# Kernel optimization log

Measured on AMD Instinct MI355X. Metric: run time of the kernel, lower is better.

Reference implementation:

```python
import jax, jax.numpy as jnp
import numpy as np

B = 128      # trees per batch
D = 10       # tree depth (perfect binary tree)
L = 2 ** D   # leaves per tree
V = 50000    # vocab
E = 300      # embed size
C = 5        # num classes


def setup_inputs() -> dict:
    key = jax.random.key(0)
    k0, k1, k2, k3 = jax.random.split(key, 4)
    return {
        "word_ids": jax.random.randint(k0, (B, L), 0, V),
        "embedding": jax.random.normal(k1, (V, E), jnp.float32) * 0.02,
        "W_w": jax.random.normal(k2, (E, 2 * E), jnp.float32) * (1.0 / np.sqrt(2 * E)),
        "W_b": jnp.zeros((E,), jnp.float32),
        "P_w": jax.random.normal(k3, (C, E), jnp.float32) * (1.0 / np.sqrt(E)),
        "P_b": jnp.zeros((C,), jnp.float32),
    }


def reference(word_ids, embedding, W_w, W_b, P_w, P_b):
    # Leaf nodes: relu(Embedding(word))  -> [B, L, E]
    h = jax.nn.relu(embedding[word_ids])
    # projection of every node (torch Linear: x @ W.T + b)
    logits = [jnp.einsum("bne,ce->bnc", h, P_w) + P_b]
    # Combine same-depth sibling pairs level by level (D fixed levels).
    for _ in range(D):
        pair = jnp.concatenate([h[:, 0::2], h[:, 1::2]], axis=-1)  # [B, n/2, 2E]
        h = jax.nn.relu(jnp.einsum("bnf,ef->bne", pair, W_w) + W_b)  # [B, n/2, E]
        logits.append(jnp.einsum("bne,ce->bnc", h, P_w) + P_b)
    # All node logits, leaves first then each internal level up to the root.
    return jnp.concatenate(logits, axis=1)  # [B, 2L-1, C]
```

## Files before the change

### kernel.cpp

```cpp
#include <hip/hip_runtime.h>
#include <hip/hip_bf16.h>

#define B_ 128
#define E_ 300
#define C_ 5
#define NODES 2047

typedef __attribute__((ext_vector_type(8))) short short8;
typedef __attribute__((ext_vector_type(4))) float f32x4;
typedef __hip_bfloat16 bf16;

__device__ __forceinline__ short f2bs(float v) {
  bf16 b = (bf16)v;
  return *reinterpret_cast<short*>(&b);
}

__device__ __forceinline__ short8 pack_relu(f32x4 v0, f32x4 v1) {
  short8 s;
#pragma unroll
  for (int j = 0; j < 4; j++) s[j] = f2bs(fmaxf(v0[j], 0.f));
#pragma unroll
  for (int j = 0; j < 4; j++) s[4 + j] = f2bs(fmaxf(v1[j], 0.f));
  return s;
}

#define HSROW(base, r) ((base) + (r) * 312)

#define PROJ_A(rowptr, ks, k0)                               \
  ((ks) == 9 && half >= 2 ? (short8){0, 0, 0, 0, 0, 0, 0, 0} \
                          : *(const short8*)((rowptr) + (k0)))

__global__ __launch_bounds__(256) void prep_k(
    const float* __restrict__ emb, const float* __restrict__ Ww,
    const float* __restrict__ Pw, bf16* __restrict__ T, bf16* __restrict__ Wf,
    bf16* __restrict__ Pqf, bf16* __restrict__ Ppf, int V) {
  int idx = blockIdx.x * 256 + threadIdx.x;
  int tchunks = V * 38;
  if (idx < tchunks) {
    int v = idx / 38, c = idx % 38;
    const float* src = emb + (size_t)v * E_ + c * 8;
    f32x4 v0 = *(const f32x4*)src;
    f32x4 v1 = (c == 37) ? (f32x4){0.f, 0.f, 0.f, 0.f}
                         : *(const f32x4*)(src + 4);
    *(short8*)(T + (size_t)v * 304 + c * 8) = pack_relu(v0, v1);
  }
  if (idx < 20 * 19 * 64) {
    int wnt = idx / 1216, rem = idx % 1216;
    int ks = rem >> 6, l = rem & 63;
    int n = wnt * 16 + (l & 15);
    int k0 = ks * 32 + (l >> 4) * 8;
    short8 v;
#pragma unroll
    for (int j = 0; j < 8; j++) {
      int k = k0 + j;
      float x = 0.f;
      if (n < E_) {
        if (k < E_) x = Ww[n * 600 + k];
        else if (k >= 304 && k < 604) x = Ww[n * 600 + k - 4];
      }
      v[j] = f2bs(x);
    }
    *(short8*)(Wf + (size_t)idx * 8) = v;
  }
  if (idx < 2 * 19 * 64) {
    int p = idx / 1216, rem = idx % 1216;
    int ks = rem >> 6, l = rem & 63;
    int q = l & 15;
    int k0 = ks * 32 + (l >> 4) * 8;
    short8 v;
#pragma unroll
    for (int j = 0; j < 8; j++) {
      int e = k0 + j - 304 * p;
      float x = (q < C_ && e >= 0 && e < E_) ? Pw[q * E_ + e] : 0.f;
      v[j] = f2bs(x);
    }
    *(short8*)(Pqf + (size_t)idx * 8) = v;
  }
  if (idx < 10 * 64) {
    int ks = idx >> 6, l = idx & 63;
    int q = l & 15;
    int k0 = ks * 32 + (l >> 4) * 8;
    short8 v;
#pragma unroll
    for (int j = 0; j < 8; j++) {
      int e = k0 + j;
      float x = (q < C_ && e < E_) ? Pw[q * E_ + e] : 0.f;
      v[j] = f2bs(x);
    }
    *(short8*)(Ppf + (size_t)idx * 8) = v;
  }
}

__global__ __launch_bounds__(256, 2) void fused_l1_k(
    const int* __restrict__ wid, const bf16* __restrict__ T,
    const bf16* __restrict__ Wf, const float* __restrict__ Wb,
    const bf16* __restrict__ Pqf, const bf16* __restrict__ Ppf,
    const float* __restrict__ Pb, bf16* __restrict__ h1f,
    float* __restrict__ out) {
  __shared__ short ldsA[64 * 616 + 64];
  int tid = threadIdx.x;
  int m0 = blockIdx.x * 64;

#pragma unroll 2
  for (int it = 0; it < 19; ++it) {
    int i = it * 256 + tid;
    int r = i / 76, c2 = i % 76;
    int par = c2 >= 38 ? 1 : 0;
    int c = c2 - 38 * par;
    int word = wid[2 * (m0 + r) + par];
    short8 v = *(const short8*)(T + (size_t)word * 304 + c * 8);
    *(short8*)&ldsA[r * 616 + par * 304 + c * 8] = v;
  }
  __syncthreads();

  int w = tid >> 6, l = tid & 63, q = l & 15, half = l >> 4;
  int ab0 = (0 * 16 + q) * 616;
  int ab1 = (1 * 16 + q) * 616;
  int ab2 = (2 * 16 + q) * 616;
  int ab3 = (3 * 16 + q) * 616;

  f32x4 acc[4][5];
#pragma unroll
  for (int rt = 0; rt < 4; rt++)
#pragma unroll
    for (int nt = 0; nt < 5; nt++) acc[rt][nt] = (f32x4){0.f, 0.f, 0.f, 0.f};
  f32x4 pacc0 = (f32x4){0.f, 0.f, 0.f, 0.f};
  f32x4 pacc1 = (f32x4){0.f, 0.f, 0.f, 0.f};

#pragma unroll 2
  for (int ks = 0; ks < 19; ks++) {
    int k0 = ks * 32 + half * 8;
    short8 a0 = *(const short8*)&ldsA[ab0 + k0];
    short8 a1 = *(const short8*)&ldsA[ab1 + k0];
    short8 a2 = *(const short8*)&ldsA[ab2 + k0];
    short8 a3 = *(const short8*)&ldsA[ab3 + k0];
    short8 al = w == 0 ? a0 : (w == 1 ? a1 : (w == 2 ? a2 : a3));
    short8 pq0 = *(const short8*)(Pqf + ((size_t)(0 * 19 + ks) * 64 + l) * 8);
    short8 pq1 = *(const short8*)(Pqf + ((size_t)(1 * 19 + ks) * 64 + l) * 8);
    pacc0 = __builtin_amdgcn_mfma_f32_16x16x32_bf16(al, pq0, pacc0, 0, 0, 0);
    pacc1 = __builtin_amdgcn_mfma_f32_16x16x32_bf16(al, pq1, pacc1, 0, 0, 0);
#pragma unroll
    for (int nt = 0; nt < 5; nt++) {
      short8 b = *(const short8*)(Wf +
          ((size_t)((5 * w + nt) * 19 + ks) * 64 + l) * 8);
      acc[0][nt] =
          __builtin_amdgcn_mfma_f32_16x16x32_bf16(a0, b, acc[0][nt], 0, 0, 0);
      acc[1][nt] =
          __builtin_amdgcn_mfma_f32_16x16x32_bf16(a1, b, acc[1][nt], 0, 0, 0);
      acc[2][nt] =
          __builtin_amdgcn_mfma_f32_16x16x32_bf16(a2, b, acc[2][nt], 0, 0, 0);
      acc[3][nt] =
          __builtin_amdgcn_mfma_f32_16x16x32_bf16(a3, b, acc[3][nt], 0, 0, 0);
    }
  }
  __syncthreads();

#pragma unroll
  for (int nt = 0; nt < 5; nt++) {
    int n = w * 80 + nt * 16 + q;
    float wb = (n < E_) ? Wb[n] : 0.f;
    if (n < 304) {
#pragma unroll
      for (int rt = 0; rt < 4; rt++)
#pragma unroll
        for (int j = 0; j < 4; j++) {
          int rl = rt * 16 + half * 4 + j;
          HSROW(ldsA, rl)[n] = f2bs(fmaxf(acc[rt][nt][j] + wb, 0.f));
        }
    }
  }
  if (q < C_) {
    float pb = Pb[q];
#pragma unroll
    for (int j = 0; j < 4; j++) {
      int row = m0 + w * 16 + half * 4 + j;
      int leaf0 = 2 * row, leaf1 = 2 * row + 1;
      out[((size_t)(leaf0 >> 10) * NODES + (leaf0 & 1023)) * C_ + q] =
          pacc0[j] + pb;
      out[((size_t)(leaf1 >> 10) * NODES + (leaf1 & 1023)) * C_ + q] =
          pacc1[j] + pb;
    }
  }
  __syncthreads();

  for (int i = tid; i < 2 * 19 * 64; i += 256) {
    int gl = i / 1216, rem = i % 1216;
    int ks = rem >> 6, ll = rem & 63;
    int qq = ll & 15, hh = ll >> 4;
    int k0 = ks * 32 + hh * 8;
    int sel = k0 >= 304 ? 1 : 0;
    int e = k0 - 304 * sel;
    int lr = 2 * (gl * 16 + qq) + sel;
    short8 v = *(const short8*)&HSROW(ldsA, lr)[e];
    *(short8*)(h1f + (((size_t)((m0 >> 5) + gl) * 19 + ks) * 64 + ll) * 8) = v;
  }
  f32x4 pc = (f32x4){0.f, 0.f, 0.f, 0.f};
#pragma unroll
  for (int ks = 0; ks < 10; ks++) {
    int k0 = ks * 32 + half * 8;
    short8 a = PROJ_A(HSROW(ldsA, 16 * w + q), ks, k0);
    short8 b = *(const short8*)(Ppf + ((size_t)ks * 64 + l) * 8);
    pc = __builtin_amdgcn_mfma_f32_16x16x32_bf16(a, b, pc, 0, 0, 0);
  }
  if (q < C_) {
    float pb = Pb[q];
#pragma unroll
    for (int j = 0; j < 4; j++) {
      int m = m0 + w * 16 + half * 4 + j;
      out[((size_t)(m >> 9) * NODES + 1024 + (m & 511)) * C_ + q] = pc[j] + pb;
    }
  }
}

template <int RT>
__global__ __launch_bounds__(256, RT == 4 ? 3 : 4) void combine_k(
    const bf16* __restrict__ hin_f, const bf16* __restrict__ Wf,
    const float* __restrict__ Wb, const bf16* __restrict__ Ppf,
    const float* __restrict__ Pb, bf16* __restrict__ hout_f,
    float* __restrict__ out, int node_off, int nshift) {
  __shared__ short hsO[RT * 16 * 312 + 64];
  int tid = threadIdx.x;
  int w = tid >> 6, l = tid & 63, q = l & 15, half = l >> 4;
  int m0 = blockIdx.x * (RT * 16);
  int g0 = m0 >> 4;

  f32x4 acc[RT][5];
#pragma unroll
  for (int rt = 0; rt < RT; rt++)
#pragma unroll
    for (int nt = 0; nt < 5; nt++) acc[rt][nt] = (f32x4){0.f, 0.f, 0.f, 0.f};

#pragma unroll 2
  for (int ks = 0; ks < 19; ks++) {
    short8 a[RT];
#pragma unroll
    for (int rt = 0; rt < RT; rt++)
      a[rt] = *(const short8*)(hin_f +
          (((size_t)(g0 + rt) * 19 + ks) * 64 + l) * 8);
#pragma unroll
    for (int nt = 0; nt < 5; nt++) {
      short8 b = *(const short8*)(Wf +
          ((size_t)((5 * w + nt) * 19 + ks) * 64 + l) * 8);
#pragma unroll
      for (int rt = 0; rt < RT; rt++)
        acc[rt][nt] = __builtin_amdgcn_mfma_f32_16x16x32_bf16(
            a[rt], b, acc[rt][nt], 0, 0, 0);
    }
  }

#pragma unroll
  for (int nt = 0; nt < 5; nt++) {
    int n = w * 80 + nt * 16 + q;
    float wb = (n < E_) ? Wb[n] : 0.f;
    if (n < 304) {
#pragma unroll
      for (int rt = 0; rt < RT; rt++)
#pragma unroll
        for (int j = 0; j < 4; j++) {
          int rl = rt * 16 + half * 4 + j;
          HSROW(hsO, rl)[n] = f2bs(fmaxf(acc[rt][nt][j] + wb, 0.f));
        }
    }
  }
  __syncthreads();

  for (int i = tid; i < (RT / 2) * 1216; i += 256) {
    int gl = i / 1216, rem = i % 1216;
    int ks = rem >> 6, ll = rem & 63;
    int qq = ll & 15, hh = ll >> 4;
    int k0 = ks * 32 + hh * 8;
    int sel = k0 >= 304 ? 1 : 0;
    int e = k0 - 304 * sel;
    int lr = 2 * (gl * 16 + qq) + sel;
    short8 v = *(const short8*)&HSROW(hsO, lr)[e];
    *(short8*)(hout_f +
               (((size_t)((m0 >> 5) + gl) * 19 + ks) * 64 + ll) * 8) = v;
  }
  if (w < RT) {
    f32x4 pacc = (f32x4){0.f, 0.f, 0.f, 0.f};
#pragma unroll
    for (int ks = 0; ks < 10; ks++) {
      int k0 = ks * 32 + half * 8;
      short8 a = PROJ_A(HSROW(hsO, 16 * w + q), ks, k0);
      short8 b = *(const short8*)(Ppf + ((size_t)ks * 64 + l) * 8);
      pacc = __builtin_amdgcn_mfma_f32_16x16x32_bf16(a, b, pacc, 0, 0, 0);
    }
    if (q < C_) {
      float pb = Pb[q];
#pragma unroll
      for (int j = 0; j < 4; j++) {
        size_t m = m0 + w * 16 + half * 4 + j;
        size_t b_ = m >> nshift;
        size_t n = m & (((size_t)1 << nshift) - 1);
        out[((size_t)b_ * NODES + node_off + n) * C_ + q] = pacc[j] + pb;
      }
    }
  }
}

extern "C" void kernel_launch(void* const* d_in, const int* in_sizes, int n_in,
                              void* d_out, int out_size, void* d_ws,
                              size_t ws_size, hipStream_t stream) {
  const int* wid = (const int*)d_in[0];
  const float* emb = (const float*)d_in[1];
  const float* Ww = (const float*)d_in[2];
  const float* Wb = (const float*)d_in[3];
  const float* Pw = (const float*)d_in[4];
  const float* Pb = (const float*)d_in[5];
  float* out = (float*)d_out;
  int V = in_sizes[1] / E_;

  bf16* hA = (bf16*)d_ws;
  bf16* hB = hA + (size_t)B_ * 512 * 304;
  bf16* Wf = hB + (size_t)B_ * 256 * 304;
  bf16* Pqf = Wf + (size_t)20 * 19 * 512;
  bf16* Ppf = Pqf + (size_t)2 * 19 * 512;
  bf16* T = Ppf + (size_t)10 * 512;

  int tchunks = V * 38;
  prep_k<<<(tchunks + 255) / 256, 256, 0, stream>>>(emb, Ww, Pw, T, Wf, Pqf,
                                                    Ppf, V);
  fused_l1_k<<<1024, 256, 0, stream>>>(wid, T, Wf, Wb, Pqf, Ppf, Pb, hA, out);
  combine_k<4><<<512, 256, 0, stream>>>(hA, Wf, Wb, Ppf, Pb, hB, out, 1536, 8);
  combine_k<4><<<256, 256, 0, stream>>>(hB, Wf, Wb, Ppf, Pb, hA, out, 1792, 7);
  combine_k<2><<<256, 256, 0, stream>>>(hA, Wf, Wb, Ppf, Pb, hB, out, 1920, 6);
  combine_k<2><<<128, 256, 0, stream>>>(hB, Wf, Wb, Ppf, Pb, hA, out, 1984, 5);
  combine_k<2><<<64, 256, 0, stream>>>(hA, Wf, Wb, Ppf, Pb, hB, out, 2016, 4);
  combine_k<2><<<32, 256, 0, stream>>>(hB, Wf, Wb, Ppf, Pb, hA, out, 2032, 3);
  combine_k<2><<<16, 256, 0, stream>>>(hA, Wf, Wb, Ppf, Pb, hB, out, 2040, 2);
  combine_k<2><<<8, 256, 0, stream>>>(hB, Wf, Wb, Ppf, Pb, hA, out, 2044, 1);
  combine_k<2><<<4, 256, 0, stream>>>(hA, Wf, Wb, Ppf, Pb, hB, out, 2046, 0);
}
```

Baseline: 212.6 us.

## Fuse tree levels pairwise into kernels, keeping intermediate level in LDS

The leaf kernel now also computes the second combine level from LDS and writes only level-2 activations. The per-level combine kernel is replaced by a dual-level kernel that computes two consecutive levels per block, with the intermediate level kept in shared memory. This cuts the launch count from ten to five and removes a global round trip of activations for every other level. In exchange, the later levels run with fewer blocks, and the second stage of each block uses only 16 rows, so MFMA utilisation and occupancy drop.

```diff
diff --git a/kernel.cpp b/kernel.cpp
--- a/kernel.cpp
+++ b/kernel.cpp
@@ -91,13 +91,14 @@
   }
 }
 
-__global__ __launch_bounds__(256, 2) void fused_l1_k(
+__global__ __launch_bounds__(256, 2) void fused_l12_k(
     const int* __restrict__ wid, const bf16* __restrict__ T,
     const bf16* __restrict__ Wf, const float* __restrict__ Wb,
     const bf16* __restrict__ Pqf, const bf16* __restrict__ Ppf,
-    const float* __restrict__ Pb, bf16* __restrict__ h1f,
+    const float* __restrict__ Pb, bf16* __restrict__ h2f,
     float* __restrict__ out) {
   __shared__ short ldsA[64 * 616 + 64];
+  short* t2 = ldsA + 20032;
   int tid = threadIdx.x;
   int m0 = blockIdx.x * 64;
 
@@ -183,68 +184,128 @@
   }
   __syncthreads();
 
-  for (int i = tid; i < 2 * 19 * 64; i += 256) {
-    int gl = i / 1216, rem = i % 1216;
-    int ks = rem >> 6, ll = rem & 63;
+  {
+    f32x4 pc = (f32x4){0.f, 0.f, 0.f, 0.f};
+#pragma unroll
+    for (int ks = 0; ks < 10; ks++) {
+      int k0 = ks * 32 + half * 8;
+      short8 a = PROJ_A(HSROW(ldsA, 16 * w + q), ks, k0);
+      short8 b = *(const short8*)(Ppf + ((size_t)ks * 64 + l) * 8);
+      pc = __builtin_amdgcn_mfma_f32_16x16x32_bf16(a, b, pc, 0, 0, 0);
+    }
+    if (q < C_) {
+      float pb = Pb[q];
+#pragma unroll
+      for (int j = 0; j < 4; j++) {
+        int m = m0 + w * 16 + half * 4 + j;
+        out[((size_t)(m >> 9) * NODES + 1024 + (m & 511)) * C_ + q] =
+            pc[j] + pb;
+      }
+    }
+  }
+
+  f32x4 acc2[2][5];
+#pragma unroll
+  for (int rt = 0; rt < 2; rt++)
+#pragma unroll
+    for (int nt = 0; nt < 5; nt++) acc2[rt][nt] = (f32x4){0.f, 0.f, 0.f, 0.f};
+#pragma unroll 2
+  for (int ks = 0; ks < 19; ks++) {
+    int k0 = ks * 32 + half * 8;
+    int sel = k0 >= 304 ? 1 : 0;
+    int e0 = k0 - 304 * sel;
+    short8 a0 = *(const short8*)&HSROW(ldsA, 2 * q + sel)[e0];
+    short8 a1 = *(const short8*)&HSROW(ldsA, 32 + 2 * q + sel)[e0];
+#pragma unroll
+    for (int nt = 0; nt < 5; nt++) {
+      short8 b = *(const short8*)(Wf +
+          ((size_t)((5 * w + nt) * 19 + ks) * 64 + l) * 8);
+      acc2[0][nt] =
+          __builtin_amdgcn_mfma_f32_16x16x32_bf16(a0, b, acc2[0][nt], 0, 0, 0);
+      acc2[1][nt] =
+          __builtin_amdgcn_mfma_f32_16x16x32_bf16(a1, b, acc2[1][nt], 0, 0, 0);
+    }
+  }
+#pragma unroll
+  for (int nt = 0; nt < 5; nt++) {
+    int n = w * 80 + nt * 16 + q;
+    float wb = (n < E_) ? Wb[n] : 0.f;
+    if (n < 304) {
+#pragma unroll
+      for (int rt = 0; rt < 2; rt++)
+#pragma unroll
+        for (int j = 0; j < 4; j++) {
+          int rl = rt * 16 + half * 4 + j;
+          HSROW(t2, rl)[n] = f2bs(fmaxf(acc2[rt][nt][j] + wb, 0.f));
+        }
+    }
+  }
+  __syncthreads();
+
+  if (w < 2) {
+    f32x4 pc = (f32x4){0.f, 0.f, 0.f, 0.f};
+#pragma unroll
+    for (int ks = 0; ks < 10; ks++) {
+      int k0 = ks * 32 + half * 8;
+      short8 a = PROJ_A(HSROW(t2, 16 * w + q), ks, k0);
+      short8 b = *(const short8*)(Ppf + ((size_t)ks * 64 + l) * 8);
+      pc = __builtin_amdgcn_mfma_f32_16x16x32_bf16(a, b, pc, 0, 0, 0);
+    }
+    if (q < C_) {
+      float pb = Pb[q];
+#pragma unroll
+      for (int j = 0; j < 4; j++) {
+        int m = blockIdx.x * 32 + w * 16 + half * 4 + j;
+        out[((size_t)(m >> 8) * NODES + 1536 + (m & 255)) * C_ + q] =
+            pc[j] + pb;
+      }
+    }
+  }
+  for (int i = tid; i < 1216; i += 256) {
+    int ks = i >> 6, ll = i & 63;
     int qq = ll & 15, hh = ll >> 4;
     int k0 = ks * 32 + hh * 8;
     int sel = k0 >= 304 ? 1 : 0;
     int e = k0 - 304 * sel;
-    int lr = 2 * (gl * 16 + qq) + sel;
-    short8 v = *(const short8*)&HSROW(ldsA, lr)[e];
-    *(short8*)(h1f + (((size_t)((m0 >> 5) + gl) * 19 + ks) * 64 + ll) * 8) = v;
-  }
-  f32x4 pc = (f32x4){0.f, 0.f, 0.f, 0.f};
-#pragma unroll
-  for (int ks = 0; ks < 10; ks++) {
-    int k0 = ks * 32 + half * 8;
-    short8 a = PROJ_A(HSROW(ldsA, 16 * w + q), ks, k0);
-    short8 b = *(const short8*)(Ppf + ((size_t)ks * 64 + l) * 8);
-    pc = __builtin_amdgcn_mfma_f32_16x16x32_bf16(a, b, pc, 0, 0, 0);
-  }
-  if (q < C_) {
-    float pb = Pb[q];
-#pragma unroll
-    for (int j = 0; j < 4; j++) {
-      int m = m0 + w * 16 + half * 4 + j;
-      out[((size_t)(m >> 9) * NODES + 1024 + (m & 511)) * C_ + q] = pc[j] + pb;
-    }
-  }
-}
-
-template <int RT>
-__global__ __launch_bounds__(256, RT == 4 ? 3 : 4) void combine_k(
+    int lr = 2 * qq + sel;
+    short8 v = *(const short8*)&HSROW(t2, lr)[e];
+    *(short8*)(h2f + (((size_t)blockIdx.x * 19 + ks) * 64 + ll) * 8) = v;
+  }
+}
+
+__global__ __launch_bounds__(256, 4) void dual_k(
     const bf16* __restrict__ hin_f, const bf16* __restrict__ Wf,
     const float* __restrict__ Wb, const bf16* __restrict__ Ppf,
     const float* __restrict__ Pb, bf16* __restrict__ hout_f,
-    float* __restrict__ out, int node_off, int nshift) {
-  __shared__ short hsO[RT * 16 * 312 + 64];
+    float* __restrict__ out, int off1, int ns1, int off2, int ns2, int last) {
+  __shared__ short lds[48 * 312 + 16];
+  short* t1 = lds;
+  short* t2 = lds + 32 * 312;
   int tid = threadIdx.x;
   int w = tid >> 6, l = tid & 63, q = l & 15, half = l >> 4;
-  int m0 = blockIdx.x * (RT * 16);
-  int g0 = m0 >> 4;
-
-  f32x4 acc[RT][5];
-#pragma unroll
-  for (int rt = 0; rt < RT; rt++)
+  int b = blockIdx.x;
+  int g0 = 2 * b;
+
+  f32x4 acc[2][5];
+#pragma unroll
+  for (int rt = 0; rt < 2; rt++)
 #pragma unroll
     for (int nt = 0; nt < 5; nt++) acc[rt][nt] = (f32x4){0.f, 0.f, 0.f, 0.f};
 
 #pragma unroll 2
   for (int ks = 0; ks < 19; ks++) {
-    short8 a[RT];
-#pragma unroll
-    for (int rt = 0; rt < RT; rt++)
-      a[rt] = *(const short8*)(hin_f +
-          (((size_t)(g0 + rt) * 19 + ks) * 64 + l) * 8);
+    short8 a0 = *(const short8*)(hin_f +
+        (((size_t)g0 * 19 + ks) * 64 + l) * 8);
+    short8 a1 = *(const short8*)(hin_f +
+        (((size_t)(g0 + 1) * 19 + ks) * 64 + l) * 8);
 #pragma unroll
     for (int nt = 0; nt < 5; nt++) {
-      short8 b = *(const short8*)(Wf +
+      short8 bfr = *(const short8*)(Wf +
           ((size_t)((5 * w + nt) * 19 + ks) * 64 + l) * 8);
-#pragma unroll
-      for (int rt = 0; rt < RT; rt++)
-        acc[rt][nt] = __builtin_amdgcn_mfma_f32_16x16x32_bf16(
-            a[rt], b, acc[rt][nt], 0, 0, 0);
+      acc[0][nt] =
+          __builtin_amdgcn_mfma_f32_16x16x32_bf16(a0, bfr, acc[0][nt], 0, 0, 0);
+      acc[1][nt] =
+          __builtin_amdgcn_mfma_f32_16x16x32_bf16(a1, bfr, acc[1][nt], 0, 0, 0);
     }
   }
 
@@ -254,45 +315,97 @@
     float wb = (n < E_) ? Wb[n] : 0.f;
     if (n < 304) {
 #pragma unroll
-      for (int rt = 0; rt < RT; rt++)
+      for (int rt = 0; rt < 2; rt++)
 #pragma unroll
         for (int j = 0; j < 4; j++) {
           int rl = rt * 16 + half * 4 + j;
-          HSROW(hsO, rl)[n] = f2bs(fmaxf(acc[rt][nt][j] + wb, 0.f));
+          HSROW(t1, rl)[n] = f2bs(fmaxf(acc[rt][nt][j] + wb, 0.f));
         }
     }
   }
   __syncthreads();
 
-  for (int i = tid; i < (RT / 2) * 1216; i += 256) {
-    int gl = i / 1216, rem = i % 1216;
-    int ks = rem >> 6, ll = rem & 63;
-    int qq = ll & 15, hh = ll >> 4;
-    int k0 = ks * 32 + hh * 8;
-    int sel = k0 >= 304 ? 1 : 0;
-    int e = k0 - 304 * sel;
-    int lr = 2 * (gl * 16 + qq) + sel;
-    short8 v = *(const short8*)&HSROW(hsO, lr)[e];
-    *(short8*)(hout_f +
-               (((size_t)((m0 >> 5) + gl) * 19 + ks) * 64 + ll) * 8) = v;
-  }
-  if (w < RT) {
+  if (w < 2) {
     f32x4 pacc = (f32x4){0.f, 0.f, 0.f, 0.f};
 #pragma unroll
     for (int ks = 0; ks < 10; ks++) {
       int k0 = ks * 32 + half * 8;
-      short8 a = PROJ_A(HSROW(hsO, 16 * w + q), ks, k0);
-      short8 b = *(const short8*)(Ppf + ((size_t)ks * 64 + l) * 8);
-      pacc = __builtin_amdgcn_mfma_f32_16x16x32_bf16(a, b, pacc, 0, 0, 0);
+      short8 a = PROJ_A(HSROW(t1, 16 * w + q), ks, k0);
+      short8 bfr = *(const short8*)(Ppf + ((size_t)ks * 64 + l) * 8);
+      pacc = __builtin_amdgcn_mfma_f32_16x16x32_bf16(a, bfr, pacc, 0, 0, 0);
     }
     if (q < C_) {
       float pb = Pb[q];
 #pragma unroll
       for (int j = 0; j < 4; j++) {
-        size_t m = m0 + w * 16 + half * 4 + j;
-        size_t b_ = m >> nshift;
-        size_t n = m & (((size_t)1 << nshift) - 1);
-        out[((size_t)b_ * NODES + node_off + n) * C_ + q] = pacc[j] + pb;
+        size_t m = (size_t)b * 32 + w * 16 + half * 4 + j;
+        out[((m >> ns1) * NODES + off1 + (m & (((size_t)1 << ns1) - 1))) * C_ +
+            q] = pacc[j] + pb;
+      }
+    }
+  }
+
+  f32x4 acc2[5];
+#pragma unroll
+  for (int nt = 0; nt < 5; nt++) acc2[nt] = (f32x4){0.f, 0.f, 0.f, 0.f};
+#pragma unroll 2
+  for (int ks = 0; ks < 19; ks++) {
+    int k0 = ks * 32 + half * 8;
+    int sel = k0 >= 304 ? 1 : 0;
+    int e0 = k0 - 304 * sel;
+    short8 a = *(const short8*)&HSROW(t1, 2 * q + sel)[e0];
+#pragma unroll
+    for (int nt = 0; nt < 5; nt++) {
+      short8 bfr = *(const short8*)(Wf +
+          ((size_t)((5 * w + nt) * 19 + ks) * 64 + l) * 8);
+      acc2[nt] =
+          __builtin_amdgcn_mfma_f32_16x16x32_bf16(a, bfr, acc2[nt], 0, 0, 0);
+    }
+  }
+#pragma unroll
+  for (int nt = 0; nt < 5; nt++) {
+    int n = w * 80 + nt * 16 + q;
+    float wb = (n < E_) ? Wb[n] : 0.f;
+    if (n < 304) {
+#pragma unroll
+      for (int j = 0; j < 4; j++) {
+        HSROW(t2, half * 4 + j)[n] = f2bs(fmaxf(acc2[nt][j] + wb, 0.f));
+      }
+    }
+  }
+  __syncthreads();
+
+  if (w == 0) {
+    f32x4 pacc = (f32x4){0.f, 0.f, 0.f, 0.f};
+#pragma unroll
+    for (int ks = 0; ks < 10; ks++) {
+      int k0 = ks * 32 + half * 8;
+      short8 a = PROJ_A(HSROW(t2, q), ks, k0);
+      short8 bfr = *(const short8*)(Ppf + ((size_t)ks * 64 + l) * 8);
+      pacc = __builtin_amdgcn_mfma_f32_16x16x32_bf16(a, bfr, pacc, 0, 0, 0);
+    }
+    if (q < C_) {
+      float pb = Pb[q];
+#pragma unroll
+      for (int j = 0; j < 4; j++) {
+        size_t m = (size_t)b * 16 + half * 4 + j;
+        out[((m >> ns2) * NODES + off2 + (m & (((size_t)1 << ns2) - 1))) * C_ +
+            q] = pacc[j] + pb;
+      }
+    }
+  }
+  if (!last) {
+    int g = b >> 1, hi = b & 1;
+    for (int i = tid; i < 1216; i += 256) {
+      int ks = i >> 6, ll = i & 63;
+      int qq = ll & 15, hh = ll >> 4;
+      if ((qq >> 3) == hi) {
+        int k0 = ks * 32 + hh * 8;
+        int sel = k0 >= 304 ? 1 : 0;
+        int e = k0 - 304 * sel;
+        int lr2 = 2 * (qq & 7) + sel;
+        short8 v = *(const short8*)&HSROW(t2, lr2)[e];
+        *(short8*)(hout_f + (((size_t)g * 19 + ks) * 64 + ll) * 8) = v;
       }
     }
   }
@@ -320,14 +433,13 @@
   int tchunks = V * 38;
   prep_k<<<(tchunks + 255) / 256, 256, 0, stream>>>(emb, Ww, Pw, T, Wf, Pqf,
                                                     Ppf, V);
-  fused_l1_k<<<1024, 256, 0, stream>>>(wid, T, Wf, Wb, Pqf, Ppf, Pb, hA, out);
-  combine_k<4><<<512, 256, 0, stream>>>(hA, Wf, Wb, Ppf, Pb, hB, out, 1536, 8);
-  combine_k<4><<<256, 256, 0, stream>>>(hB, Wf, Wb, Ppf, Pb, hA, out, 1792, 7);
-  combine_k<2><<<256, 256, 0, stream>>>(hA, Wf, Wb, Ppf, Pb, hB, out, 1920, 6);
-  combine_k<2><<<128, 256, 0, stream>>>(hB, Wf, Wb, Ppf, Pb, hA, out, 1984, 5);
-  combine_k<2><<<64, 256, 0, stream>>>(hA, Wf, Wb, Ppf, Pb, hB, out, 2016, 4);
-  combine_k<2><<<32, 256, 0, stream>>>(hB, Wf, Wb, Ppf, Pb, hA, out, 2032, 3);
-  combine_k<2><<<16, 256, 0, stream>>>(hA, Wf, Wb, Ppf, Pb, hB, out, 2040, 2);
-  combine_k<2><<<8, 256, 0, stream>>>(hB, Wf, Wb, Ppf, Pb, hA, out, 2044, 1);
-  combine_k<2><<<4, 256, 0, stream>>>(hA, Wf, Wb, Ppf, Pb, hB, out, 2046, 0);
-}
+  fused_l12_k<<<1024, 256, 0, stream>>>(wid, T, Wf, Wb, Pqf, Ppf, Pb, hB, out);
+  dual_k<<<512, 256, 0, stream>>>(hB, Wf, Wb, Ppf, Pb, hA, out,
+                                  1792, 7, 1920, 6, 0);
+  dual_k<<<128, 256, 0, stream>>>(hA, Wf, Wb, Ppf, Pb, hB, out,
+                                  1984, 5, 2016, 4, 0);
+  dual_k<<<32, 256, 0, stream>>>(hB, Wf, Wb, Ppf, Pb, hA, out,
+                                 2032, 3, 2040, 2, 0);
+  dual_k<<<8, 256, 0, stream>>>(hA, Wf, Wb, Ppf, Pb, hB, out,
+                                2044, 1, 2046, 0, 1);
+}
```

After: 389.1 us. 1.83x slower.

## Double block size to 512 threads, splitting row tiles across two wave groups

Applied to the files above, without the earlier changes.

Every kernel now runs with 8 waves per block instead of 4. The two groups of four waves each compute half of the row tiles against the same weight columns, and the leaf projection work is also split between them. The goal is to raise waves per block and cut per-wave accumulator registers, which improves latency hiding, especially for the small late levels with few blocks. The cost is that each weight fragment is now loaded from global memory by twice as many waves, and launch_bounds changes affect register allocation.

```diff
diff --git a/kernel.cpp b/kernel.cpp
--- a/kernel.cpp
+++ b/kernel.cpp
@@ -91,7 +91,7 @@
   }
 }
 
-__global__ __launch_bounds__(256, 2) void fused_l1_k(
+__global__ __launch_bounds__(512, 2) void fused_l1_k(
     const int* __restrict__ wid, const bf16* __restrict__ T,
     const bf16* __restrict__ Wf, const float* __restrict__ Wb,
     const bf16* __restrict__ Pqf, const bf16* __restrict__ Ppf,
@@ -101,9 +101,7 @@
   int tid = threadIdx.x;
   int m0 = blockIdx.x * 64;
 
-#pragma unroll 2
-  for (int it = 0; it < 19; ++it) {
-    int i = it * 256 + tid;
+  for (int i = tid; i < 64 * 76; i += 512) {
     int r = i / 76, c2 = i % 76;
     int par = c2 >= 38 ? 1 : 0;
     int c = c2 - 38 * par;
@@ -114,57 +112,49 @@
   __syncthreads();
 
   int w = tid >> 6, l = tid & 63, q = l & 15, half = l >> 4;
-  int ab0 = (0 * 16 + q) * 616;
-  int ab1 = (1 * 16 + q) * 616;
-  int ab2 = (2 * 16 + q) * 616;
-  int ab3 = (3 * 16 + q) * 616;
-
-  f32x4 acc[4][5];
-#pragma unroll
-  for (int rt = 0; rt < 4; rt++)
+  int wg = w & 3, wh = w >> 2;
+  int ab0 = ((wh * 2 + 0) * 16 + q) * 616;
+  int ab1 = ((wh * 2 + 1) * 16 + q) * 616;
+  int abL = ((w & 3) * 16 + q) * 616;
+  int pL = w >> 2;
+
+  f32x4 acc[2][5];
+#pragma unroll
+  for (int rt = 0; rt < 2; rt++)
 #pragma unroll
     for (int nt = 0; nt < 5; nt++) acc[rt][nt] = (f32x4){0.f, 0.f, 0.f, 0.f};
-  f32x4 pacc0 = (f32x4){0.f, 0.f, 0.f, 0.f};
-  f32x4 pacc1 = (f32x4){0.f, 0.f, 0.f, 0.f};
+  f32x4 pacc = (f32x4){0.f, 0.f, 0.f, 0.f};
 
 #pragma unroll 2
   for (int ks = 0; ks < 19; ks++) {
     int k0 = ks * 32 + half * 8;
     short8 a0 = *(const short8*)&ldsA[ab0 + k0];
     short8 a1 = *(const short8*)&ldsA[ab1 + k0];
-    short8 a2 = *(const short8*)&ldsA[ab2 + k0];
-    short8 a3 = *(const short8*)&ldsA[ab3 + k0];
-    short8 al = w == 0 ? a0 : (w == 1 ? a1 : (w == 2 ? a2 : a3));
-    short8 pq0 = *(const short8*)(Pqf + ((size_t)(0 * 19 + ks) * 64 + l) * 8);
-    short8 pq1 = *(const short8*)(Pqf + ((size_t)(1 * 19 + ks) * 64 + l) * 8);
-    pacc0 = __builtin_amdgcn_mfma_f32_16x16x32_bf16(al, pq0, pacc0, 0, 0, 0);
-    pacc1 = __builtin_amdgcn_mfma_f32_16x16x32_bf16(al, pq1, pacc1, 0, 0, 0);
+    short8 al = *(const short8*)&ldsA[abL + k0];
+    short8 pq = *(const short8*)(Pqf + ((size_t)(pL * 19 + ks) * 64 + l) * 8);
+    pacc = __builtin_amdgcn_mfma_f32_16x16x32_bf16(al, pq, pacc, 0, 0, 0);
 #pragma unroll
     for (int nt = 0; nt < 5; nt++) {
       short8 b = *(const short8*)(Wf +
-          ((size_t)((5 * w + nt) * 19 + ks) * 64 + l) * 8);
+          ((size_t)((5 * wg + nt) * 19 + ks) * 64 + l) * 8);
       acc[0][nt] =
           __builtin_amdgcn_mfma_f32_16x16x32_bf16(a0, b, acc[0][nt], 0, 0, 0);
       acc[1][nt] =
           __builtin_amdgcn_mfma_f32_16x16x32_bf16(a1, b, acc[1][nt], 0, 0, 0);
-      acc[2][nt] =
-          __builtin_amdgcn_mfma_f32_16x16x32_bf16(a2, b, acc[2][nt], 0, 0, 0);
-      acc[3][nt] =
-          __builtin_amdgcn_mfma_f32_16x16x32_bf16(a3, b, acc[3][nt], 0, 0, 0);
     }
   }
   __syncthreads();
 
 #pragma unroll
   for (int nt = 0; nt < 5; nt++) {
-    int n = w * 80 + nt * 16 + q;
+    int n = wg * 80 + nt * 16 + q;
     float wb = (n < E_) ? Wb[n] : 0.f;
     if (n < 304) {
 #pragma unroll
-      for (int rt = 0; rt < 4; rt++)
+      for (int rt = 0; rt < 2; rt++)
 #pragma unroll
         for (int j = 0; j < 4; j++) {
-          int rl = rt * 16 + half * 4 + j;
+          int rl = (wh * 2 + rt) * 16 + half * 4 + j;
           HSROW(ldsA, rl)[n] = f2bs(fmaxf(acc[rt][nt][j] + wb, 0.f));
         }
     }
@@ -173,17 +163,15 @@
     float pb = Pb[q];
 #pragma unroll
     for (int j = 0; j < 4; j++) {
-      int row = m0 + w * 16 + half * 4 + j;
-      int leaf0 = 2 * row, leaf1 = 2 * row + 1;
-      out[((size_t)(leaf0 >> 10) * NODES + (leaf0 & 1023)) * C_ + q] =
-          pacc0[j] + pb;
-      out[((size_t)(leaf1 >> 10) * NODES + (leaf1 & 1023)) * C_ + q] =
-          pacc1[j] + pb;
+      int row = m0 + (w & 3) * 16 + half * 4 + j;
+      int leaf = 2 * row + pL;
+      out[((size_t)(leaf >> 10) * NODES + (leaf & 1023)) * C_ + q] =
+          pacc[j] + pb;
     }
   }
   __syncthreads();
 
-  for (int i = tid; i < 2 * 19 * 64; i += 256) {
+  for (int i = tid; i < 2 * 19 * 64; i += 512) {
     int gl = i / 1216, rem = i % 1216;
     int ks = rem >> 6, ll = rem & 63;
     int qq = ll & 15, hh = ll >> 4;
@@ -194,55 +182,60 @@
     short8 v = *(const short8*)&HSROW(ldsA, lr)[e];
     *(short8*)(h1f + (((size_t)((m0 >> 5) + gl) * 19 + ks) * 64 + ll) * 8) = v;
   }
-  f32x4 pc = (f32x4){0.f, 0.f, 0.f, 0.f};
-#pragma unroll
-  for (int ks = 0; ks < 10; ks++) {
-    int k0 = ks * 32 + half * 8;
-    short8 a = PROJ_A(HSROW(ldsA, 16 * w + q), ks, k0);
-    short8 b = *(const short8*)(Ppf + ((size_t)ks * 64 + l) * 8);
-    pc = __builtin_amdgcn_mfma_f32_16x16x32_bf16(a, b, pc, 0, 0, 0);
-  }
-  if (q < C_) {
-    float pb = Pb[q];
-#pragma unroll
-    for (int j = 0; j < 4; j++) {
-      int m = m0 + w * 16 + half * 4 + j;
-      out[((size_t)(m >> 9) * NODES + 1024 + (m & 511)) * C_ + q] = pc[j] + pb;
+  if (w < 4) {
+    f32x4 pc = (f32x4){0.f, 0.f, 0.f, 0.f};
+#pragma unroll
+    for (int ks = 0; ks < 10; ks++) {
+      int k0 = ks * 32 + half * 8;
+      short8 a = PROJ_A(HSROW(ldsA, 16 * w + q), ks, k0);
+      short8 b = *(const short8*)(Ppf + ((size_t)ks * 64 + l) * 8);
+      pc = __builtin_amdgcn_mfma_f32_16x16x32_bf16(a, b, pc, 0, 0, 0);
+    }
+    if (q < C_) {
+      float pb = Pb[q];
+#pragma unroll
+      for (int j = 0; j < 4; j++) {
+        int m = m0 + w * 16 + half * 4 + j;
+        out[((size_t)(m >> 9) * NODES + 1024 + (m & 511)) * C_ + q] =
+            pc[j] + pb;
+      }
     }
   }
 }
 
 template <int RT>
-__global__ __launch_bounds__(256, RT == 4 ? 3 : 4) void combine_k(
+__global__ __launch_bounds__(512, 2) void combine_k(
     const bf16* __restrict__ hin_f, const bf16* __restrict__ Wf,
     const float* __restrict__ Wb, const bf16* __restrict__ Ppf,
     const float* __restrict__ Pb, bf16* __restrict__ hout_f,
     float* __restrict__ out, int node_off, int nshift) {
+  const int HR = RT / 2;
   __shared__ short hsO[RT * 16 * 312 + 64];
   int tid = threadIdx.x;
   int w = tid >> 6, l = tid & 63, q = l & 15, half = l >> 4;
+  int wg = w & 3, wh = w >> 2;
   int m0 = blockIdx.x * (RT * 16);
-  int g0 = m0 >> 4;
-
-  f32x4 acc[RT][5];
-#pragma unroll
-  for (int rt = 0; rt < RT; rt++)
+  int g0 = (m0 >> 4) + wh * HR;
+
+  f32x4 acc[HR][5];
+#pragma unroll
+  for (int rt = 0; rt < HR; rt++)
 #pragma unroll
     for (int nt = 0; nt < 5; nt++) acc[rt][nt] = (f32x4){0.f, 0.f, 0.f, 0.f};
 
 #pragma unroll 2
   for (int ks = 0; ks < 19; ks++) {
-    short8 a[RT];
-#pragma unroll
-    for (int rt = 0; rt < RT; rt++)
+    short8 a[HR];
+#pragma unroll
+    for (int rt = 0; rt < HR; rt++)
       a[rt] = *(const short8*)(hin_f +
           (((size_t)(g0 + rt) * 19 + ks) * 64 + l) * 8);
 #pragma unroll
     for (int nt = 0; nt < 5; nt++) {
       short8 b = *(const short8*)(Wf +
-          ((size_t)((5 * w + nt) * 19 + ks) * 64 + l) * 8);
-#pragma unroll
-      for (int rt = 0; rt < RT; rt++)
+          ((size_t)((5 * wg + nt) * 19 + ks) * 64 + l) * 8);
+#pragma unroll
+      for (int rt = 0; rt < HR; rt++)
         acc[rt][nt] = __builtin_amdgcn_mfma_f32_16x16x32_bf16(
             a[rt], b, acc[rt][nt], 0, 0, 0);
     }
@@ -250,21 +243,21 @@
 
 #pragma unroll
   for (int nt = 0; nt < 5; nt++) {
-    int n = w * 80 + nt * 16 + q;
+    int n = wg * 80 + nt * 16 + q;
     float wb = (n < E_) ? Wb[n] : 0.f;
     if (n < 304) {
 #pragma unroll
-      for (int rt = 0; rt < RT; rt++)
+      for (int rt = 0; rt < HR; rt++)
 #pragma unroll
         for (int j = 0; j < 4; j++) {
-          int rl = rt * 16 + half * 4 + j;
+          int rl = (wh * HR + rt) * 16 + half * 4 + j;
           HSROW(hsO, rl)[n] = f2bs(fmaxf(acc[rt][nt][j] + wb, 0.f));
         }
     }
   }
   __syncthreads();
 
-  for (int i = tid; i < (RT / 2) * 1216; i += 256) {
+  for (int i = tid; i < (RT / 2) * 1216; i += 512) {
     int gl = i / 1216, rem = i % 1216;
     int ks = rem >> 6, ll = rem & 63;
     int qq = ll & 15, hh = ll >> 4;
@@ -320,14 +313,14 @@
   int tchunks = V * 38;
   prep_k<<<(tchunks + 255) / 256, 256, 0, stream>>>(emb, Ww, Pw, T, Wf, Pqf,
                                                     Ppf, V);
-  fused_l1_k<<<1024, 256, 0, stream>>>(wid, T, Wf, Wb, Pqf, Ppf, Pb, hA, out);
-  combine_k<4><<<512, 256, 0, stream>>>(hA, Wf, Wb, Ppf, Pb, hB, out, 1536, 8);
-  combine_k<4><<<256, 256, 0, stream>>>(hB, Wf, Wb, Ppf, Pb, hA, out, 1792, 7);
-  combine_k<2><<<256, 256, 0, stream>>>(hA, Wf, Wb, Ppf, Pb, hB, out, 1920, 6);
-  combine_k<2><<<128, 256, 0, stream>>>(hB, Wf, Wb, Ppf, Pb, hA, out, 1984, 5);
-  combine_k<2><<<64, 256, 0, stream>>>(hA, Wf, Wb, Ppf, Pb, hB, out, 2016, 4);
-  combine_k<2><<<32, 256, 0, stream>>>(hB, Wf, Wb, Ppf, Pb, hA, out, 2032, 3);
-  combine_k<2><<<16, 256, 0, stream>>>(hA, Wf, Wb, Ppf, Pb, hB, out, 2040, 2);
-  combine_k<2><<<8, 256, 0, stream>>>(hB, Wf, Wb, Ppf, Pb, hA, out, 2044, 1);
-  combine_k<2><<<4, 256, 0, stream>>>(hA, Wf, Wb, Ppf, Pb, hB, out, 2046, 0);
-}
+  fused_l1_k<<<1024, 512, 0, stream>>>(wid, T, Wf, Wb, Pqf, Ppf, Pb, hA, out);
+  combine_k<4><<<512, 512, 0, stream>>>(hA, Wf, Wb, Ppf, Pb, hB, out, 1536, 8);
+  combine_k<4><<<256, 512, 0, stream>>>(hB, Wf, Wb, Ppf, Pb, hA, out, 1792, 7);
+  combine_k<2><<<256, 512, 0, stream>>>(hA, Wf, Wb, Ppf, Pb, hB, out, 1920, 6);
+  combine_k<2><<<128, 512, 0, stream>>>(hB, Wf, Wb, Ppf, Pb, hA, out, 1984, 5);
+  combine_k<2><<<64, 512, 0, stream>>>(hA, Wf, Wb, Ppf, Pb, hB, out, 2016, 4);
+  combine_k<2><<<32, 512, 0, stream>>>(hB, Wf, Wb, Ppf, Pb, hA, out, 2032, 3);
+  combine_k<2><<<16, 512, 0, stream>>>(hA, Wf, Wb, Ppf, Pb, hB, out, 2040, 2);
+  combine_k<2><<<8, 512, 0, stream>>>(hB, Wf, Wb, Ppf, Pb, hA, out, 2044, 1);
+  combine_k<2><<<4, 512, 0, stream>>>(hA, Wf, Wb, Ppf, Pb, hB, out, 2046, 0);
+}
```

Result: faster. 202.7 us, median of 3 (-4.6%).
